# Optimization experiments

Measured on AMD Instinct MI355X. Metric: run time of the kernel, lower is better.

Reference implementation:

```python
import jax, jax.numpy as jnp
import numpy as np

N_H = 16
N_KV = 4
D_K = 128
ROPE_BASE = 10000.0


def _rope(t, cos, sin):
    # t: [B, T, H, d_k]; cos/sin: [1, T, 1, d_k//2]
    te, to = t[..., 0::2], t[..., 1::2]
    oe = te * cos - to * sin
    oo = te * sin + to * cos
    return jnp.stack([oe, oo], axis=-1).reshape(t.shape)


def setup_inputs() -> dict:
    key = jax.random.key(0)
    ks = jax.random.split(key, 5)
    B, T, d = 4, 2048, 2048
    s = 0.02
    return {
        "x": jax.random.normal(ks[0], (B, T, d), jnp.float32),
        "Wq": jax.random.normal(ks[1], (d, d), jnp.float32) * s,
        "Wk": jax.random.normal(ks[2], (d, N_KV * D_K), jnp.float32) * s,
        "Wv": jax.random.normal(ks[3], (d, N_KV * D_K), jnp.float32) * s,
        "Wp": jax.random.normal(ks[4], (d, d), jnp.float32) * s,
        "bp": jnp.zeros((d,), jnp.float32),
    }


def reference(x, Wq, Wk, Wv, Wp, bp):
    B, T, C = x.shape
    g = N_H // N_KV  # group size

    q = (x @ Wq).reshape(B, T, N_H, D_K)
    k = (x @ Wk).reshape(B, T, N_KV, D_K)
    v = (x @ Wv).reshape(B, T, N_KV, D_K)

    # RoPE frequencies (constants)
    theta = ROPE_BASE ** (-2.0 * jnp.arange(0, D_K, 2, dtype=jnp.float32) / D_K)
    freq = jnp.arange(T, dtype=jnp.float32)[:, None] * theta[None, :]  # [T, d_k//2]
    cos = jnp.cos(freq)[None, :, None, :]
    sin = jnp.sin(freq)[None, :, None, :]
    q = _rope(q, cos, sin)
    k = _rope(k, cos, sin)

    # GQA: group q heads by shared kv head (equiv to repeat_interleave on kv)
    q = q.reshape(B, T, N_KV, g, D_K).transpose(0, 2, 3, 1, 4)  # [B,n_kv,g,T,d_k]
    k = k.transpose(0, 2, 1, 3)  # [B,n_kv,T,d_k]
    v = v.transpose(0, 2, 1, 3)

    scores = jnp.einsum('bngqd,bnkd->bngqk', q, k) * (D_K ** -0.5)
    causal = jnp.tril(jnp.ones((T, T), bool))
    scores = jnp.where(causal, scores, -jnp.inf)
    attn = jax.nn.softmax(scores, axis=-1)
    out = jnp.einsum('bngqk,bnkd->bngqd', attn, v)  # [B,n_kv,g,T,d_k]
    out = out.transpose(0, 3, 1, 2, 4).reshape(B, T, C)
    return out @ Wp + bp
```

## Files before the change

### kernel.cpp

```cpp
#include <hip/hip_runtime.h>
#include <hip/hip_bf16.h>
#include <math.h>

typedef __bf16 bf16_t;
typedef __bf16 bf16x8 __attribute__((ext_vector_type(8)));
typedef __bf16 bf16x4 __attribute__((ext_vector_type(4)));
typedef float f32x4 __attribute__((ext_vector_type(4)));
typedef float f32x16 __attribute__((ext_vector_type(16)));
typedef unsigned int u32;

#define MFMA16 __builtin_amdgcn_mfma_f32_16x16x32_bf16
#define MFMA32 __builtin_amdgcn_mfma_f32_32x32x16_bf16

static __device__ __forceinline__ u32 pkbf(float a, float b) {
  union { bf16_t h[2]; u32 u; } z;
  z.h[0] = (bf16_t)a; z.h[1] = (bf16_t)b;
  return z.u;
}

static __device__ __forceinline__ void gload16(const bf16_t* g, bf16_t* l) {
  __builtin_amdgcn_global_load_lds(
      (const __attribute__((address_space(1))) void*)g,
      (__attribute__((address_space(3))) void*)l, 16, 0, 0);
}

__global__ void k_f32_to_bf16(const float* __restrict__ in, bf16_t* __restrict__ out, long n) {
  long i = ((long)blockIdx.x * blockDim.x + threadIdx.x) * 4;
  long stride = (long)gridDim.x * blockDim.x * 4;
  for (; i < n; i += stride) {
    const float4 v = *(const float4*)(in + i);
    bf16x4 o; o[0] = (bf16_t)v.x; o[1] = (bf16_t)v.y; o[2] = (bf16_t)v.z; o[3] = (bf16_t)v.w;
    *(bf16x4*)(out + i) = o;
  }
}

__global__ void k_transpose_bf16(const float* __restrict__ W, bf16_t* __restrict__ WT,
                                 int K, int N) {
  __shared__ float tile[32][33];
  int n0 = blockIdx.x * 32, k0 = blockIdx.y * 32;
  int tx = threadIdx.x & 31, ty = threadIdx.x >> 5;
#pragma unroll
  for (int i = 0; i < 4; i++)
    tile[ty + i * 8][tx] = W[(size_t)(k0 + ty + i * 8) * N + n0 + tx];
  __syncthreads();
#pragma unroll
  for (int i = 0; i < 4; i++) {
    int n = ty + i * 8;
    WT[(size_t)(n0 + n) * K + k0 + tx] = (bf16_t)tile[tx][n];
  }
}

__global__ void k_rope(bf16_t* __restrict__ qkv) {
  int idx = blockIdx.x * blockDim.x + threadIdx.x;
  if (idx >= 8192 * 1280) return;
  int r = idx / 1280, p = idx - r * 1280;
  int t = r & 2047;
  int i = p & 63;
  float theta = exp2f(-(float)i * 0.41524101186092029f);
  float f = (float)t * theta;
  float s, c;
  sincosf(f, &s, &c);
  bf16_t* a = qkv + (size_t)r * 3072 + p * 2;
  float e = (float)a[0], o = (float)a[1];
  a[0] = (bf16_t)(e * c - o * s);
  a[1] = (bf16_t)(e * s + o * c);
}

template <bool F32OUT>
__global__ __launch_bounds__(256, 2) void k_gemm_bt(
    const bf16_t* __restrict__ A, const bf16_t* __restrict__ BT,
    bf16_t* __restrict__ Cb, float* __restrict__ Cf,
    const float* __restrict__ bias, int M, int N, int K, int nwg) {
  __shared__ bf16_t sA[128 * 64];
  __shared__ bf16_t sB[128 * 64];
  int nbn = N >> 7;
  int orig = (int)blockIdx.x;
  int swz = (orig & 7) * (nwg >> 3) + (orig >> 3);
  int bm = swz / nbn, bn = swz % nbn;
  int tid = threadIdx.x;
  int lane = tid & 63, wid = tid >> 6;
  int wm = (wid >> 1) << 6, wn = (wid & 1) << 6;
  int lr = lane & 15, lq = lane >> 4;
  f32x4 acc[4][4] = {};

  int srow = wid * 32 + (lane >> 3);
  int scol = (lane & 7) * 8;
  const bf16_t* Ag = A + (size_t)(bm * 128 + srow) * K + scol;
  const bf16_t* Bg = BT + (size_t)(bn * 128 + srow) * K + scol;
  bf16_t* Al = &sA[(wid * 32) * 64];
  bf16_t* Bl = &sB[(wid * 32) * 64];

  for (int k0 = 0; k0 < K; k0 += 64) {
#pragma unroll
    for (int i = 0; i < 4; i++) {
      gload16(Ag + (size_t)i * 8 * K + k0, Al + i * 8 * 64);
      gload16(Bg + (size_t)i * 8 * K + k0, Bl + i * 8 * 64);
    }
    __syncthreads();
#pragma unroll
    for (int kc = 0; kc < 2; kc++) {
      bf16x8 af[4], bfr[4];
#pragma unroll
      for (int m = 0; m < 4; m++)
        af[m] = *(const bf16x8*)&sA[(wm + m * 16 + lr) * 64 + kc * 32 + lq * 8];
#pragma unroll
      for (int n = 0; n < 4; n++)
        bfr[n] = *(const bf16x8*)&sB[(wn + n * 16 + lr) * 64 + kc * 32 + lq * 8];
#pragma unroll
      for (int m = 0; m < 4; m++)
#pragma unroll
        for (int n = 0; n < 4; n++)
          acc[m][n] = MFMA16(af[m], bfr[n], acc[m][n], 0, 0, 0);
    }
    __syncthreads();
  }
#pragma unroll
  for (int m = 0; m < 4; m++) {
    int row0 = bm * 128 + wm + m * 16 + lq * 4;
#pragma unroll
    for (int n = 0; n < 4; n++) {
      int col = bn * 128 + wn + n * 16 + lr;
#pragma unroll
      for (int r = 0; r < 4; r++) {
        if constexpr (F32OUT)
          Cf[(size_t)(row0 + r) * N + col] = acc[m][n][r] + bias[col];
        else
          Cb[(size_t)(row0 + r) * N + col] = (bf16_t)acc[m][n][r];
      }
    }
  }
}

__global__ __launch_bounds__(256, 2) void k_attn(const bf16_t* __restrict__ qkv,
                                                 bf16_t* __restrict__ out) {
  __shared__ bf16_t sK[64 * 128];
  __shared__ bf16_t sVT[128 * 72];
  int bid = blockIdx.x;
  int g = bid >> 6;
  int qt = (g & 1) ? (g >> 1) : (15 - (g >> 1));
  int bh = bid & 63;
  int h = bh & 15, b = bh >> 4;
  int kvh = h >> 2;
  const size_t RS = 3072;
  const bf16_t* Qb = qkv + (size_t)b * 2048 * RS + h * 128;
  const bf16_t* Kb = qkv + (size_t)b * 2048 * RS + 2048 + kvh * 128;
  const bf16_t* Vb = Kb + 512;
  int q0 = qt * 128;
  int tid = threadIdx.x, lane = tid & 63, wid = tid >> 6;
  int l31 = lane & 31, hi = lane >> 5;
  int qw = q0 + wid * 32;

  bf16x8 qf[8];
  {
    const bf16_t* qrow = Qb + (size_t)(qw + l31) * RS + hi * 8;
#pragma unroll
    for (int dc = 0; dc < 8; dc++)
      qf[dc] = *(const bf16x8*)(qrow + dc * 16);
  }

  f32x16 oT[4] = {};
  float m_r = -INFINITY, l_r = 0.f;
  const float SC = 0.08838834764831845f * 1.4426950408889634f;

  int k_row = tid >> 4, k_seg = tid & 15;
  int vc = tid & 127, vro = (tid >> 7) * 8;

  bf16x8 kreg[4], vreg[4];
  auto issue = [&](int k0) {
#pragma unroll
    for (int ps = 0; ps < 4; ps++)
      kreg[ps] = *(const bf16x8*)(Kb + (size_t)(k0 + k_row + ps * 16) * RS + k_seg * 8);
#pragma unroll
    for (int i = 0; i < 4; i++) {
      int kr = vro + i * 16;
#pragma unroll
      for (int j = 0; j < 8; j++)
        vreg[i][j] = Vb[(size_t)(k0 + kr + j) * RS + vc];
    }
  };

  int ntiles = 2 * qt + 2;
  issue(0);
  for (int kt = 0; kt < ntiles; kt++) {
    int k0 = kt * 64;
#pragma unroll
    for (int ps = 0; ps < 4; ps++) {
      int row = k_row + ps * 16;
      int off = row * 256 + ((k_seg * 16) ^ ((row & 7) << 4));
      *(bf16x8*)((char*)sK + off) = kreg[ps];
    }
#pragma unroll
    for (int i = 0; i < 4; i++)
      *(bf16x8*)&sVT[vc * 72 + vro + i * 16] = vreg[i];
    __syncthreads();
    if (kt + 1 < ntiles) issue(k0 + 64);

    if (k0 <= qw + 31) {
      f32x16 sa0 = {}, sa1 = {};
      __builtin_amdgcn_s_setprio(1);
#pragma unroll
      for (int dc = 0; dc < 8; dc++) {
        int cb = (dc * 32 + hi * 16) ^ ((l31 & 7) << 4);
        bf16x8 kf0 = *(const bf16x8*)((const char*)sK + l31 * 256 + cb);
        bf16x8 kf1 = *(const bf16x8*)((const char*)sK + (32 + l31) * 256 + cb);
        sa0 = MFMA32(kf0, qf[dc], sa0, 0, 0, 0);
        sa1 = MFMA32(kf1, qf[dc], sa1, 0, 0, 0);
      }
      __builtin_amdgcn_s_setprio(0);
      float p[2][16];
      int qg = qw + l31;
      if (k0 + 63 <= qw) {
#pragma unroll
        for (int r = 0; r < 16; r++) { p[0][r] = sa0[r]; p[1][r] = sa1[r]; }
      } else {
#pragma unroll
        for (int nf = 0; nf < 2; nf++)
#pragma unroll
          for (int r = 0; r < 16; r++) {
            int kg = k0 + nf * 32 + (r & 3) + 8 * (r >> 2) + 4 * hi;
            p[nf][r] = (kg <= qg) ? (nf ? sa1[r] : sa0[r]) : -INFINITY;
          }
      }
      float mx[16];
#pragma unroll
      for (int r = 0; r < 16; r++) mx[r] = fmaxf(p[0][r], p[1][r]);
#pragma unroll
      for (int s = 8; s >= 1; s >>= 1)
#pragma unroll
        for (int r = 0; r < 8; r++)
          if (r < s) mx[r] = fmaxf(mx[r], mx[r + s]);
      float pm = mx[0] * SC;
      pm = fmaxf(pm, __shfl_xor(pm, 32));
      bool skip = __all(pm <= m_r + 8.f);
      float mn = skip ? m_r : fmaxf(m_r, pm);
      float alpha = skip ? 1.f : exp2f(m_r - mn);
      m_r = mn;
      float nm = -m_r;
#pragma unroll
      for (int nf = 0; nf < 2; nf++)
#pragma unroll
        for (int r = 0; r < 16; r++)
          p[nf][r] = exp2f(fmaf(p[nf][r], SC, nm));
      float sm[16];
#pragma unroll
      for (int r = 0; r < 16; r++) sm[r] = p[0][r] + p[1][r];
#pragma unroll
      for (int s = 8; s >= 1; s >>= 1)
#pragma unroll
        for (int r = 0; r < 8; r++)
          if (r < s) sm[r] += sm[r + s];
      float rs = sm[0] + __shfl_xor(sm[0], 32);
      l_r = l_r * alpha + rs;
      if (!skip) {
#pragma unroll
        for (int c = 0; c < 4; c++)
#pragma unroll
          for (int r = 0; r < 16; r++) oT[c][r] *= alpha;
      }
#pragma unroll
      for (int nf = 0; nf < 2; nf++) {
        u32 Qk[4][2];
#pragma unroll
        for (int gg = 0; gg < 4; gg++) {
          Qk[gg][0] = pkbf(p[nf][4 * gg + 0], p[nf][4 * gg + 1]);
          Qk[gg][1] = pkbf(p[nf][4 * gg + 2], p[nf][4 * gg + 3]);
        }
#pragma unroll
        for (int kc = 0; kc < 2; kc++) {
          u32 x0 = __shfl_xor(Qk[2 * kc + 1 - hi][0], 32);
          u32 x1 = __shfl_xor(Qk[2 * kc + 1 - hi][1], 32);
          u32 o0 = Qk[2 * kc + hi][0], o1 = Qk[2 * kc + hi][1];
          union { u32 w[4]; bf16x8 v; } pf;
          pf.w[0] = hi ? x0 : o0;
          pf.w[1] = hi ? x1 : o1;
          pf.w[2] = hi ? o0 : x0;
          pf.w[3] = hi ? o1 : x1;
          int slot = nf * 2 + kc;
          __builtin_amdgcn_s_setprio(1);
#pragma unroll
          for (int c = 0; c < 4; c++) {
            bf16x8 vf = *(const bf16x8*)&sVT[(c * 32 + l31) * 72 + slot * 16 + hi * 8];
            oT[c] = MFMA32(vf, pf.v, oT[c], 0, 0, 0);
          }
          __builtin_amdgcn_s_setprio(0);
        }
      }
    }
    __syncthreads();
  }
  float inv = 1.f / l_r;
  size_t row = (size_t)b * 2048 + qw + l31;
#pragma unroll
  for (int c = 0; c < 4; c++)
#pragma unroll
    for (int rr = 0; rr < 4; rr++) {
      bf16x4 o4;
#pragma unroll
      for (int j = 0; j < 4; j++) o4[j] = (bf16_t)(oT[c][rr * 4 + j] * inv);
      *(bf16x4*)(out + row * 2048 + h * 128 + c * 32 + rr * 8 + hi * 4) = o4;
    }
}

extern "C" void kernel_launch(void* const* d_in, const int* in_sizes, int n_in,
                              void* d_out, int out_size, void* d_ws, size_t ws_size,
                              hipStream_t stream) {
  const float* x = (const float*)d_in[0];
  const float* Wq = (const float*)d_in[1];
  const float* Wk = (const float*)d_in[2];
  const float* Wv = (const float*)d_in[3];
  const float* Wp = (const float*)d_in[4];
  const float* bp = (const float*)d_in[5];
  float* out = (float*)d_out;

  bf16_t* ws = (bf16_t*)d_ws;
  bf16_t* xb = ws;
  bf16_t* qkv = ws + 16777216;
  bf16_t* WqkvT = ws + 16777216 + 25165824;
  bf16_t* WpT = WqkvT + 6291456;

  k_f32_to_bf16<<<2048, 256, 0, stream>>>(x, xb, 16777216L);
  k_transpose_bf16<<<dim3(64, 64), 256, 0, stream>>>(Wq, WqkvT, 2048, 2048);
  k_transpose_bf16<<<dim3(16, 64), 256, 0, stream>>>(Wk, WqkvT + (size_t)2048 * 2048, 2048, 512);
  k_transpose_bf16<<<dim3(16, 64), 256, 0, stream>>>(Wv, WqkvT + (size_t)2560 * 2048, 2048, 512);
  k_transpose_bf16<<<dim3(64, 64), 256, 0, stream>>>(Wp, WpT, 2048, 2048);

  k_gemm_bt<false><<<64 * 24, 256, 0, stream>>>(xb, WqkvT, qkv, nullptr, nullptr, 8192, 3072, 2048, 64 * 24);
  k_rope<<<40960, 256, 0, stream>>>(qkv);
  k_attn<<<1024, 256, 0, stream>>>(qkv, xb);
  k_gemm_bt<true><<<64 * 16, 256, 0, stream>>>(xb, WpT, nullptr, out, bp, 8192, 2048, 2048, 64 * 16);
}
```

Before: 433.8 us.

## Pre-transpose V into a global VT buffer and vectorize attention V loads

```diff
diff --git a/kernel.cpp b/kernel.cpp
--- a/kernel.cpp
+++ b/kernel.cpp
@@ -48,6 +48,21 @@
     int n = ty + i * 8;
     WT[(size_t)(n0 + n) * K + k0 + tx] = (bf16_t)tile[tx][n];
   }
+}
+
+__global__ void k_build_vt(const bf16_t* __restrict__ qkv, bf16_t* __restrict__ VT) {
+  __shared__ bf16_t tile[32][33];
+  int t0 = blockIdx.x * 32, c0 = blockIdx.y * 32, b = blockIdx.z;
+  int tx = threadIdx.x & 31, ty = threadIdx.x >> 5;
+  const bf16_t* src = qkv + (size_t)b * 2048 * 3072 + 2560;
+#pragma unroll
+  for (int i = 0; i < 4; i++)
+    tile[ty + i * 8][tx] = src[(size_t)(t0 + ty + i * 8) * 3072 + c0 + tx];
+  __syncthreads();
+  bf16_t* dst = VT + (size_t)b * 512 * 2048;
+#pragma unroll
+  for (int i = 0; i < 4; i++)
+    dst[(size_t)(c0 + ty + i * 8) * 2048 + t0 + tx] = tile[tx][ty + i * 8];
 }
 
 __global__ void k_rope(bf16_t* __restrict__ qkv) {
@@ -67,7 +82,7 @@
 }
 
 template <bool F32OUT>
-__global__ __launch_bounds__(256, 2) void k_gemm_bt(
+__global__ __launch_bounds__(256, 3) void k_gemm_bt(
     const bf16_t* __restrict__ A, const bf16_t* __restrict__ BT,
     bf16_t* __restrict__ Cb, float* __restrict__ Cf,
     const float* __restrict__ bias, int M, int N, int K, int nwg) {
@@ -131,10 +146,11 @@
   }
 }
 
-__global__ __launch_bounds__(256, 2) void k_attn(const bf16_t* __restrict__ qkv,
+__global__ __launch_bounds__(256, 4) void k_attn(const bf16_t* __restrict__ qkv,
+                                                 const bf16_t* __restrict__ VT,
                                                  bf16_t* __restrict__ out) {
   __shared__ bf16_t sK[64 * 128];
-  __shared__ bf16_t sVT[128 * 72];
+  __shared__ bf16_t sVT[128 * 64];
   int bid = blockIdx.x;
   int g = bid >> 6;
   int qt = (g & 1) ? (g >> 1) : (15 - (g >> 1));
@@ -144,7 +160,7 @@
   const size_t RS = 3072;
   const bf16_t* Qb = qkv + (size_t)b * 2048 * RS + h * 128;
   const bf16_t* Kb = qkv + (size_t)b * 2048 * RS + 2048 + kvh * 128;
-  const bf16_t* Vb = Kb + 512;
+  const bf16_t* Vt = VT + (size_t)(b * 4 + kvh) * 128 * 2048;
   int q0 = qt * 128;
   int tid = threadIdx.x, lane = tid & 63, wid = tid >> 6;
   int l31 = lane & 31, hi = lane >> 5;
@@ -163,7 +179,7 @@
   const float SC = 0.08838834764831845f * 1.4426950408889634f;
 
   int k_row = tid >> 4, k_seg = tid & 15;
-  int vc = tid & 127, vro = (tid >> 7) * 8;
+  int vd = tid >> 3, vk = (tid & 7) * 8;
 
   bf16x8 kreg[4], vreg[4];
   auto issue = [&](int k0) {
@@ -171,12 +187,8 @@
     for (int ps = 0; ps < 4; ps++)
       kreg[ps] = *(const bf16x8*)(Kb + (size_t)(k0 + k_row + ps * 16) * RS + k_seg * 8);
 #pragma unroll
-    for (int i = 0; i < 4; i++) {
-      int kr = vro + i * 16;
-#pragma unroll
-      for (int j = 0; j < 8; j++)
-        vreg[i][j] = Vb[(size_t)(k0 + kr + j) * RS + vc];
-    }
+    for (int ps = 0; ps < 4; ps++)
+      vreg[ps] = *(const bf16x8*)(Vt + (size_t)(vd + ps * 32) * 2048 + k0 + vk);
   };
 
   int ntiles = 2 * qt + 2;
@@ -190,8 +202,11 @@
       *(bf16x8*)((char*)sK + off) = kreg[ps];
     }
 #pragma unroll
-    for (int i = 0; i < 4; i++)
-      *(bf16x8*)&sVT[vc * 72 + vro + i * 16] = vreg[i];
+    for (int ps = 0; ps < 4; ps++) {
+      int d = vd + ps * 32;
+      int off = d * 128 + ((vk * 2) ^ ((d & 7) << 4));
+      *(bf16x8*)((char*)sVT + off) = vreg[ps];
+    }
     __syncthreads();
     if (kt + 1 < ntiles) issue(k0 + 64);
 
@@ -276,10 +291,11 @@
           pf.w[2] = hi ? o0 : x0;
           pf.w[3] = hi ? o1 : x1;
           int slot = nf * 2 + kc;
+          int vb = (slot * 32 + hi * 16) ^ ((l31 & 7) << 4);
           __builtin_amdgcn_s_setprio(1);
 #pragma unroll
           for (int c = 0; c < 4; c++) {
-            bf16x8 vf = *(const bf16x8*)&sVT[(c * 32 + l31) * 72 + slot * 16 + hi * 8];
+            bf16x8 vf = *(const bf16x8*)((const char*)sVT + (c * 32 + l31) * 128 + vb);
             oT[c] = MFMA32(vf, pf.v, oT[c], 0, 0, 0);
           }
           __builtin_amdgcn_s_setprio(0);
@@ -317,6 +333,7 @@
   bf16_t* qkv = ws + 16777216;
   bf16_t* WqkvT = ws + 16777216 + 25165824;
   bf16_t* WpT = WqkvT + 6291456;
+  bf16_t* VT = WqkvT;
 
   k_f32_to_bf16<<<2048, 256, 0, stream>>>(x, xb, 16777216L);
   k_transpose_bf16<<<dim3(64, 64), 256, 0, stream>>>(Wq, WqkvT, 2048, 2048);
@@ -326,6 +343,7 @@
 
   k_gemm_bt<false><<<64 * 24, 256, 0, stream>>>(xb, WqkvT, qkv, nullptr, nullptr, 8192, 3072, 2048, 64 * 24);
   k_rope<<<40960, 256, 0, stream>>>(qkv);
-  k_attn<<<1024, 256, 0, stream>>>(qkv, xb);
+  k_build_vt<<<dim3(64, 16, 4), 256, 0, stream>>>(qkv, VT);
+  k_attn<<<1024, 256, 0, stream>>>(qkv, VT, xb);
   k_gemm_bt<true><<<64 * 16, 256, 0, stream>>>(xb, WpT, nullptr, out, bp, 8192, 2048, 2048, 64 * 16);
 }
```

After: 704.3 us. 1.62x slower.
